# Kernel tuning notes

Measured on AMD Instinct MI355X. Metric: run time of the kernel, lower is better.

Reference implementation:

```python
import jax, jax.numpy as jnp
import numpy as np

B, DZ, DE, M, H = 4096, 2048, 128, 32, 1024
GATE_TEMP = 1.0


def setup_inputs() -> dict:
    key = jax.random.key(0)
    ks = jax.random.split(key, 6)
    s = lambda k, shape, sc: jax.random.normal(k, shape, dtype=jnp.float32) * sc
    return dict(
        z=s(ks[0], (B, DZ), 1.0),
        base_W=s(ks[1], (3, DZ), 0.02),
        base_b=jnp.zeros((3,), jnp.float32),
        gate_W=s(ks[2], (DE, DZ), 0.02),
        gate_b=jnp.zeros((DE,), jnp.float32),
        E=s(ks[3], (M, DE), 0.02),              # material embedding table
        W1=s(ks[4], (M, H, DZ + DE), 0.02),     # stacked first-layer weights
        b1=jnp.zeros((M, H), jnp.float32),
        W2=s(ks[5], (M, 3, H), 0.02),           # stacked second-layer weights
        b2=jnp.zeros((M, 3), jnp.float32),
    )


def _l2norm(x, eps=1e-12):
    # matches F.normalize(dim=-1): x / max(||x||_2, eps)
    n = jnp.linalg.norm(x, axis=-1, keepdims=True)
    return x / jnp.maximum(n, eps)


def reference(z, base_W, base_b, gate_W, gate_b, E, W1, b1, W2, b2):
    dz = z.shape[1]
    # base head: [B, 3]
    b = z @ base_W.T + base_b
    # gate similarities (routing logits): [B, M]
    q = _l2norm(z @ gate_W.T + gate_b)
    sims = q @ _l2norm(E).T
    # Per-material 2-layer MLP on cat([z, E_m]) fused as grouped GEMMs.
    # Split W1 into the z-part and embedding-part of the concat input.
    W1z, W1e = W1[:, :, :dz], W1[:, :, dz:]
    emb_term = jnp.einsum('me,mhe->mh', E, W1e)        # [M, H], shared across batch
    h = jax.nn.gelu(
        jnp.einsum('bi,mhi->bmh', z, W1z) + emb_term[None] + b1[None],
        approximate=False,
    )                                                   # [B, M, H]
    delta = jnp.einsum('bmh,moh->bmo', h, W2) + b2[None]  # [B, M, 3]
    # scale_delta_by_gate=False path; dropout inactive at inference.
    L = (b[:, None, :] + delta).reshape(z.shape[0], -1)   # [B, 3*M]
    return L, sims
```

## Files before the change

kernel.cpp:

```cpp
#include <hip/hip_runtime.h>
#include <hip/hip_bf16.h>
#include <math.h>

#define B_ROWS 4096
#define DZ     2048
#define DE     128
#define M_EXP  32
#define H_DIM  1024
#define NBIG   32768
#define NEXTRA 256
#define NTOT   (NBIG + NEXTRA)
#define W1_LD  (DZ + DE)

typedef _Float16 half8 __attribute__((ext_vector_type(8)));
typedef float    f32x4 __attribute__((ext_vector_type(4)));

#define AS1 __attribute__((address_space(1)))
#define AS3 __attribute__((address_space(3)))

__device__ __forceinline__ void async_copy16(const void* g, void* l) {
  __builtin_amdgcn_global_load_lds((const AS1 void*)g, (AS3 void*)l, 16, 0, 0);
}

__device__ __forceinline__ half8 cvt8(const float4& a, const float4& b) {
  half8 h = {(_Float16)a.x, (_Float16)a.y, (_Float16)a.z, (_Float16)a.w,
             (_Float16)b.x, (_Float16)b.y, (_Float16)b.z, (_Float16)b.w};
  return h;
}

__device__ __forceinline__ float gelu_f(float x) {
  float u = fabsf(x) * 0.70710678118654752f;
  float t = 1.0f / fmaf(0.3275911f, u, 1.0f);
  float poly = t * fmaf(t, fmaf(t, fmaf(t, fmaf(t, 1.061405429f, -1.453152027f),
                                        1.421413741f), -0.284496736f), 0.254829592f);
  float er = 1.0f - poly * __expf(-u * u);
  er = copysignf(er, x);
  return 0.5f * x * (1.0f + er);
}

__global__ __launch_bounds__(256) void k_cvt_z(const float* __restrict__ z,
                                               _Float16* __restrict__ zpk) {
  long g = (long)blockIdx.x * 256 + threadIdx.x;
  int row = (int)(g >> 8);
  int k0  = ((int)g & 255) * 8;
  float4 a = *(const float4*)(z + (long)row * DZ + k0);
  float4 b = *(const float4*)(z + (long)row * DZ + k0 + 4);
  int r16 = row >> 4, rl = row & 15, kt = k0 >> 5, lg = (k0 >> 3) & 3;
  long dst = ((long)(r16 * 64 + kt) << 9) + (rl + 16 * lg) * 8;
  *(half8*)(zpk + dst) = cvt8(a, b);
}

__global__ __launch_bounds__(256) void k_cvt_w1(const float* __restrict__ W1,
                                                const float* __restrict__ E,
                                                const float* __restrict__ b1,
                                                _Float16* __restrict__ W1h,
                                                float* __restrict__ hbias) {
  const long n = blockIdx.x;
  const int  t = threadIdx.x;
  const float* src = W1 + n * W1_LD;
  float4 a = *(const float4*)(src + t * 8);
  float4 b = *(const float4*)(src + t * 8 + 4);
  *(half8*)(W1h + n * DZ + t * 8) = cvt8(a, b);
  if (t < 32) {
    int m = (int)(n >> 10);
    float4 w = *(const float4*)(src + DZ + t * 4);
    float4 e = *(const float4*)(E + m * DE + t * 4);
    float p = w.x * e.x + w.y * e.y + w.z * e.z + w.w * e.w;
    p += __shfl_xor(p, 16);
    p += __shfl_xor(p, 8);
    p += __shfl_xor(p, 4);
    p += __shfl_xor(p, 2);
    p += __shfl_xor(p, 1);
    if (t == 0) hbias[n] = p + b1[n];
  }
}

__global__ __launch_bounds__(256) void k_cvt_small(const float* __restrict__ gate_W,
                                                   const float* __restrict__ base_W,
                                                   _Float16* __restrict__ W1h) {
  int r = blockIdx.x;
  int t = threadIdx.x;
  const float* src = nullptr;
  if (r < 128)       src = gate_W + (long)r * DZ;
  else if (r < 131)  src = base_W + (long)(r - 128) * DZ;
  _Float16* dst = W1h + (long)(NBIG + r) * DZ + t * 8;
  if (src) {
    float4 a = *(const float4*)(src + t * 8);
    float4 b = *(const float4*)(src + t * 8 + 4);
    *(half8*)dst = cvt8(a, b);
  } else {
    half8 zv = {(_Float16)0, (_Float16)0, (_Float16)0, (_Float16)0,
                (_Float16)0, (_Float16)0, (_Float16)0, (_Float16)0};
    *(half8*)dst = zv;
  }
}

__global__ __launch_bounds__(256, 2) void k_gemm(const _Float16* __restrict__ Apk,
                                                 const _Float16* __restrict__ Bm,
                                                 const float* __restrict__ hbias,
                                                 const float* __restrict__ W2,
                                                 float* __restrict__ Lout,
                                                 float* __restrict__ qraw) {
  __shared__ _Float16 sm[3][8192];

  int flat = blockIdx.y * gridDim.x + blockIdx.x;
  int wg   = (flat & 7) * 516 + (flat >> 3);
  const int tN = wg >> 5;
  const int tM = wg & 31;

  const int tid = threadIdx.x;
  const int w = tid >> 6, l = tid & 63;
  const int wm = w >> 1, wn = w & 1;
  const int rl = l & 15, lg = l >> 4;

  const int srow  = tid >> 2;
  const int sgoff = ((tid & 3) ^ ((srow >> 1) & 3)) * 8;
  const _Float16* gB = Bm + (long)(tN * 256 + srow) * DZ + sgoff;

#define STAGE_B(sb, kt) do { \
    async_copy16(gB + (kt) * 32,            &sm[sb][tid * 8]); \
    async_copy16(gB + 64 * DZ + (kt) * 32,  &sm[sb][2048 + tid * 8]); \
    async_copy16(gB + 128 * DZ + (kt) * 32, &sm[sb][4096 + tid * 8]); \
    async_copy16(gB + 192 * DZ + (kt) * 32, &sm[sb][6144 + tid * 8]); } while (0)

  const _Float16* gA = Apk + ((long)(tM * 8 + wm * 4) << 9) * 64 + l * 8;

#define RD_AG(dst, kt) do { _Pragma("unroll") for (int _i = 0; _i < 4; ++_i) \
    dst[_i] = *(const half8*)(gA + ((long)(_i * 64 + (kt)) << 9)); } while (0)

  const int aswz  = (lg ^ ((rl >> 1) & 3)) * 8;
  const int offB0 = (wn * 128 + rl) * 32 + aswz;

  half8 AFe[4], AFo[4], bf03[4], bf47[4];
  f32x4 acc[4][8];
  f32x4 z4 = {0.f, 0.f, 0.f, 0.f};
#pragma unroll
  for (int i = 0; i < 4; ++i)
#pragma unroll
    for (int j = 0; j < 8; ++j) acc[i][j] = z4;

#define RD_B(sl) do { \
    _Pragma("unroll") for (int _j = 0; _j < 4; ++_j) \
      bf03[_j] = *(const half8*)&sm[sl][offB0 + _j * 512]; \
    _Pragma("unroll") for (int _j = 0; _j < 4; ++_j) \
      bf47[_j] = *(const half8*)&sm[sl][offB0 + (4 + _j) * 512]; } while (0)

#define MFMA32(af_) do { \
    _Pragma("unroll") for (int _i = 0; _i < 4; ++_i) \
    _Pragma("unroll") for (int _j = 0; _j < 4; ++_j) \
      acc[_i][_j] = __builtin_amdgcn_mfma_f32_16x16x32_f16(af_[_i], bf03[_j], acc[_i][_j], 0, 0, 0); \
    _Pragma("unroll") for (int _i = 0; _i < 4; ++_i) \
    _Pragma("unroll") for (int _j = 0; _j < 4; ++_j) \
      acc[_i][4 + _j] = __builtin_amdgcn_mfma_f32_16x16x32_f16(af_[_i], bf47[_j], acc[_i][4 + _j], 0, 0, 0); \
  } while (0)

#define BAR() do { asm volatile("" ::: "memory"); __builtin_amdgcn_s_barrier(); asm volatile("" ::: "memory"); } while (0)
#define VM8 asm volatile("s_waitcnt vmcnt(8)" ::: "memory")
#define VM4 asm volatile("s_waitcnt vmcnt(4)" ::: "memory")
#define VM0 asm volatile("s_waitcnt vmcnt(0)" ::: "memory")

#define TILE_FULL(sl, s2, kt2, AFc, AFn, ktA) do { \
    BAR(); \
    RD_B(sl); \
    STAGE_B(s2, kt2); \
    RD_AG(AFn, ktA); \
    VM8; \
    MFMA32(AFc); } while (0)
#define TILE_A(sl, AFc, AFn, ktA, CERT) do { \
    BAR(); \
    RD_B(sl); \
    RD_AG(AFn, ktA); \
    CERT; \
    MFMA32(AFc); } while (0)
#define TILE_LAST(sl, AFc) do { \
    BAR(); \
    RD_B(sl); \
    VM0; \
    MFMA32(AFc); } while (0)

  STAGE_B(0, 0);
  STAGE_B(1, 1);
  RD_AG(AFe, 0);
  VM8;

#pragma unroll 1
  for (int n = 0; n < 10; ++n) {
    const int t6 = 6 * n;
    TILE_FULL(0, 2, t6 + 2, AFe, AFo, t6 + 1);
    TILE_FULL(1, 0, t6 + 3, AFo, AFe, t6 + 2);
    TILE_FULL(2, 1, t6 + 4, AFe, AFo, t6 + 3);
    TILE_FULL(0, 2, t6 + 5, AFo, AFe, t6 + 4);
    TILE_FULL(1, 0, t6 + 6, AFe, AFo, t6 + 5);
    TILE_FULL(2, 1, t6 + 7, AFo, AFe, t6 + 6);
  }
  TILE_FULL(0, 2, 62, AFe, AFo, 61);
  TILE_FULL(1, 0, 63, AFo, AFe, 62);
  TILE_A(2, AFe, AFo, 63, VM4);
  TILE_LAST(0, AFo);

  if (tN < 128) {
    const int m = tN >> 2;
    float hb[8], w2v[3][8];
#pragma unroll
    for (int j = 0; j < 8; ++j) {
      int gcol = tN * 256 + wn * 128 + j * 16 + rl;
      int he   = gcol & (H_DIM - 1);
      hb[j] = hbias[gcol];
#pragma unroll
      for (int o = 0; o < 3; ++o) w2v[o][j] = W2[((long)m * 3 + o) * H_DIM + he];
    }
#pragma unroll
    for (int i = 0; i < 4; ++i) {
      const int growb = tM * 128 + wm * 64 + i * 16 + lg * 4;
#pragma unroll
      for (int r = 0; r < 4; ++r) {
        int grow = growb + r;
        float hv[8];
#pragma unroll
        for (int j = 0; j < 8; ++j) hv[j] = gelu_f(acc[i][j][r] + hb[j]);
#pragma unroll
        for (int o = 0; o < 3; ++o) {
          float p = 0.f;
#pragma unroll
          for (int j = 0; j < 8; ++j) p = fmaf(hv[j], w2v[o][j], p);
          p += __shfl_xor(p, 1);
          p += __shfl_xor(p, 2);
          p += __shfl_xor(p, 4);
          p += __shfl_xor(p, 8);
          if (rl == o) atomicAdd(&Lout[(long)grow * 96 + m * 3 + o], p);
        }
      }
    }
  } else {
#pragma unroll
    for (int i = 0; i < 4; ++i) {
      const int growb = tM * 128 + wm * 64 + i * 16 + lg * 4;
#pragma unroll
      for (int r = 0; r < 4; ++r) {
        int grow = growb + r;
        int c0 = wn * 128 + rl;
#pragma unroll
        for (int j = 0; j < 8; ++j)
          qraw[(long)grow * 256 + c0 + j * 16] = acc[i][j][r];
      }
    }
  }
}

__global__ __launch_bounds__(128) void k_post(const float* __restrict__ qraw,
                                              const float* __restrict__ gate_b,
                                              const float* __restrict__ base_b,
                                              const float* __restrict__ E,
                                              const float* __restrict__ b2,
                                              float* __restrict__ out) {
  const int b = blockIdx.x;
  const int t = threadIdx.x;
  __shared__ float qs[DE];
  __shared__ float invE[M_EXP];
  __shared__ float wsum[2];
  __shared__ float pA[M_EXP], pB[M_EXP];

  if (t < 32) {
    float ss = 0.f;
    const float* er = E + t * DE;
    for (int e = 0; e < DE; ++e) { float v = er[e]; ss += v * v; }
    invE[t] = 1.0f / fmaxf(sqrtf(ss), 1e-12f);
  }

  float val = qraw[(long)b * 256 + t] + gate_b[t];
  float ss = val * val;
  ss += __shfl_xor(ss, 1);  ss += __shfl_xor(ss, 2);  ss += __shfl_xor(ss, 4);
  ss += __shfl_xor(ss, 8);  ss += __shfl_xor(ss, 16); ss += __shfl_xor(ss, 32);
  if ((t & 63) == 0) wsum[t >> 6] = ss;
  __syncthreads();
  float inv = 1.0f / fmaxf(sqrtf(wsum[0] + wsum[1]), 1e-12f);
  qs[t] = val * inv;
  __syncthreads();

  {
    int m = t & 31, hf = t >> 5;
    const float* er = E + m * DE + hf * 32;
    const float* qq = qs + hf * 32;
    float p = 0.f;
#pragma unroll
    for (int e = 0; e < 32; ++e) p += qq[e] * er[e];
    p += __shfl_xor(p, 32);
    if (t < 32) pA[m] = p;
    else if (t >= 64 && t < 96) pB[m] = p;
    __syncthreads();
    if (t < 32) out[(long)B_ROWS * 96 + (long)b * 32 + t] = (pA[t] + pB[t]) * invE[t];
  }

  if (t < 96) {
    int o = t % 3;
    float bv = qraw[(long)b * 256 + 128 + o] + base_b[o];
    out[(long)b * 96 + t] += bv + b2[t];
  }
}

extern "C" void kernel_launch(void* const* d_in, const int* in_sizes, int n_in,
                              void* d_out, int out_size, void* d_ws, size_t ws_size,
                              hipStream_t stream) {
  const float* z      = (const float*)d_in[0];
  const float* base_W = (const float*)d_in[1];
  const float* base_b = (const float*)d_in[2];
  const float* gate_W = (const float*)d_in[3];
  const float* gate_b = (const float*)d_in[4];
  const float* E      = (const float*)d_in[5];
  const float* W1     = (const float*)d_in[6];
  const float* b1     = (const float*)d_in[7];
  const float* W2     = (const float*)d_in[8];
  const float* b2     = (const float*)d_in[9];
  float* out = (float*)d_out;

  char* ws = (char*)d_ws;
  const size_t off_zh    = 0;
  const size_t off_w1h   = off_zh  + (size_t)B_ROWS * DZ * 2;
  const size_t off_hbias = off_w1h + (size_t)NTOT * DZ * 2;
  const size_t off_qraw  = off_hbias + (size_t)NBIG * 4;
  _Float16* zpk   = (_Float16*)(ws + off_zh);
  _Float16* W1h   = (_Float16*)(ws + off_w1h);
  float*    hbias = (float*)(ws + off_hbias);
  float*    qraw  = (float*)(ws + off_qraw);

  hipMemsetAsync(d_out, 0, (size_t)B_ROWS * 96 * sizeof(float), stream);

  k_cvt_z<<<(B_ROWS * DZ) / (256 * 8), 256, 0, stream>>>(z, zpk);
  k_cvt_w1<<<NBIG, 256, 0, stream>>>(W1, E, b1, W1h, hbias);
  k_cvt_small<<<NEXTRA, 256, 0, stream>>>(gate_W, base_W, W1h);
  k_gemm<<<dim3(129, 32), 256, 0, stream>>>(zpk, W1h, hbias, W2, out, qraw);
  k_post<<<B_ROWS, 128, 0, stream>>>(qraw, gate_b, base_b, E, b2, out);
}
```

Before: 761.3 us.

## Change warp tiling to 1x4 so each warp covers all 128 rows and 64 columns

```diff
diff --git a/kernel.cpp b/kernel.cpp
--- a/kernel.cpp
+++ b/kernel.cpp
@@ -109,8 +109,8 @@
   const int tM = wg & 31;
 
   const int tid = threadIdx.x;
-  const int w = tid >> 6, l = tid & 63;
-  const int wm = w >> 1, wn = w & 1;
+  const int wn = tid >> 6;
+  const int l = tid & 63;
   const int rl = l & 15, lg = l >> 4;
 
   const int srow  = tid >> 2;
@@ -123,48 +123,42 @@
     async_copy16(gB + 128 * DZ + (kt) * 32, &sm[sb][4096 + tid * 8]); \
     async_copy16(gB + 192 * DZ + (kt) * 32, &sm[sb][6144 + tid * 8]); } while (0)
 
-  const _Float16* gA = Apk + ((long)(tM * 8 + wm * 4) << 9) * 64 + l * 8;
-
-#define RD_AG(dst, kt) do { _Pragma("unroll") for (int _i = 0; _i < 4; ++_i) \
+  const _Float16* gA = Apk + (((long)(tM * 8)) << 9) * 64 + l * 8;
+
+#define RD_AG(dst, kt) do { _Pragma("unroll") for (int _i = 0; _i < 8; ++_i) \
     dst[_i] = *(const half8*)(gA + ((long)(_i * 64 + (kt)) << 9)); } while (0)
 
   const int aswz  = (lg ^ ((rl >> 1) & 3)) * 8;
-  const int offB0 = (wn * 128 + rl) * 32 + aswz;
-
-  half8 AFe[4], AFo[4], bf03[4], bf47[4];
-  f32x4 acc[4][8];
+  const int offB0 = (wn * 64 + rl) * 32 + aswz;
+
+  half8 AFe[8], AFo[8], bf[4];
+  f32x4 acc[8][4];
   f32x4 z4 = {0.f, 0.f, 0.f, 0.f};
 #pragma unroll
-  for (int i = 0; i < 4; ++i)
-#pragma unroll
-    for (int j = 0; j < 8; ++j) acc[i][j] = z4;
-
-#define RD_B(sl) do { \
+  for (int i = 0; i < 8; ++i)
+#pragma unroll
+    for (int j = 0; j < 4; ++j) acc[i][j] = z4;
+
+#define RD_B(sl) do { _Pragma("unroll") for (int _j = 0; _j < 4; ++_j) \
+    bf[_j] = *(const half8*)&sm[sl][offB0 + _j * 512]; } while (0)
+
+#define MFMA32(af_) do { \
+    _Pragma("unroll") for (int _i = 0; _i < 8; ++_i) \
     _Pragma("unroll") for (int _j = 0; _j < 4; ++_j) \
-      bf03[_j] = *(const half8*)&sm[sl][offB0 + _j * 512]; \
-    _Pragma("unroll") for (int _j = 0; _j < 4; ++_j) \
-      bf47[_j] = *(const half8*)&sm[sl][offB0 + (4 + _j) * 512]; } while (0)
-
-#define MFMA32(af_) do { \
-    _Pragma("unroll") for (int _i = 0; _i < 4; ++_i) \
-    _Pragma("unroll") for (int _j = 0; _j < 4; ++_j) \
-      acc[_i][_j] = __builtin_amdgcn_mfma_f32_16x16x32_f16(af_[_i], bf03[_j], acc[_i][_j], 0, 0, 0); \
-    _Pragma("unroll") for (int _i = 0; _i < 4; ++_i) \
-    _Pragma("unroll") for (int _j = 0; _j < 4; ++_j) \
-      acc[_i][4 + _j] = __builtin_amdgcn_mfma_f32_16x16x32_f16(af_[_i], bf47[_j], acc[_i][4 + _j], 0, 0, 0); \
+      acc[_i][_j] = __builtin_amdgcn_mfma_f32_16x16x32_f16(af_[_i], bf[_j], acc[_i][_j], 0, 0, 0); \
   } while (0)
 
 #define BAR() do { asm volatile("" ::: "memory"); __builtin_amdgcn_s_barrier(); asm volatile("" ::: "memory"); } while (0)
-#define VM8 asm volatile("s_waitcnt vmcnt(8)" ::: "memory")
-#define VM4 asm volatile("s_waitcnt vmcnt(4)" ::: "memory")
-#define VM0 asm volatile("s_waitcnt vmcnt(0)" ::: "memory")
+#define VM12 asm volatile("s_waitcnt vmcnt(12)" ::: "memory")
+#define VM8  asm volatile("s_waitcnt vmcnt(8)" ::: "memory")
+#define VM0  asm volatile("s_waitcnt vmcnt(0)" ::: "memory")
 
 #define TILE_FULL(sl, s2, kt2, AFc, AFn, ktA) do { \
     BAR(); \
     RD_B(sl); \
     STAGE_B(s2, kt2); \
     RD_AG(AFn, ktA); \
-    VM8; \
+    VM12; \
     MFMA32(AFc); } while (0)
 #define TILE_A(sl, AFc, AFn, ktA, CERT) do { \
     BAR(); \
@@ -181,7 +175,7 @@
   STAGE_B(0, 0);
   STAGE_B(1, 1);
   RD_AG(AFe, 0);
-  VM8;
+  VM12;
 
 #pragma unroll 1
   for (int n = 0; n < 10; ++n) {
@@ -195,34 +189,32 @@
   }
   TILE_FULL(0, 2, 62, AFe, AFo, 61);
   TILE_FULL(1, 0, 63, AFo, AFe, 62);
-  TILE_A(2, AFe, AFo, 63, VM4);
+  TILE_A(2, AFe, AFo, 63, VM8);
   TILE_LAST(0, AFo);
 
   if (tN < 128) {
     const int m = tN >> 2;
-    float hb[8], w2v[3][8];
-#pragma unroll
-    for (int j = 0; j < 8; ++j) {
-      int gcol = tN * 256 + wn * 128 + j * 16 + rl;
+    float hb[4], w2v[3][4];
+#pragma unroll
+    for (int j = 0; j < 4; ++j) {
+      int gcol = tN * 256 + wn * 64 + j * 16 + rl;
       int he   = gcol & (H_DIM - 1);
       hb[j] = hbias[gcol];
 #pragma unroll
       for (int o = 0; o < 3; ++o) w2v[o][j] = W2[((long)m * 3 + o) * H_DIM + he];
     }
 #pragma unroll
-    for (int i = 0; i < 4; ++i) {
-      const int growb = tM * 128 + wm * 64 + i * 16 + lg * 4;
+    for (int i = 0; i < 8; ++i) {
+      const int growb = tM * 128 + i * 16 + lg * 4;
 #pragma unroll
       for (int r = 0; r < 4; ++r) {
         int grow = growb + r;
-        float hv[8];
-#pragma unroll
-        for (int j = 0; j < 8; ++j) hv[j] = gelu_f(acc[i][j][r] + hb[j]);
+        float hv[4];
+#pragma unroll
+        for (int j = 0; j < 4; ++j) hv[j] = gelu_f(acc[i][j][r] + hb[j]);
 #pragma unroll
         for (int o = 0; o < 3; ++o) {
-          float p = 0.f;
-#pragma unroll
-          for (int j = 0; j < 8; ++j) p = fmaf(hv[j], w2v[o][j], p);
+          float p = hv[0] * w2v[o][0] + hv[1] * w2v[o][1] + hv[2] * w2v[o][2] + hv[3] * w2v[o][3];
           p += __shfl_xor(p, 1);
           p += __shfl_xor(p, 2);
           p += __shfl_xor(p, 4);
@@ -233,14 +225,14 @@
     }
   } else {
 #pragma unroll
-    for (int i = 0; i < 4; ++i) {
-      const int growb = tM * 128 + wm * 64 + i * 16 + lg * 4;
+    for (int i = 0; i < 8; ++i) {
+      const int growb = tM * 128 + i * 16 + lg * 4;
 #pragma unroll
       for (int r = 0; r < 4; ++r) {
         int grow = growb + r;
-        int c0 = wn * 128 + rl;
-#pragma unroll
-        for (int j = 0; j < 8; ++j)
+        int c0 = wn * 64 + rl;
+#pragma unroll
+        for (int j = 0; j < 4; ++j)
           qraw[(long)grow * 256 + c0 + j * 16] = acc[i][j][r];
       }
     }
```

Measured after the change: 862.5 us. +13.3%, slower.

## Pre-pack W1 into MFMA fragment layout and drop LDS staging in GEMM

Applied to the files above, without the earlier changes.

```diff
diff --git a/kernel.cpp b/kernel.cpp
--- a/kernel.cpp
+++ b/kernel.cpp
@@ -14,13 +14,6 @@
 
 typedef _Float16 half8 __attribute__((ext_vector_type(8)));
 typedef float    f32x4 __attribute__((ext_vector_type(4)));
-
-#define AS1 __attribute__((address_space(1)))
-#define AS3 __attribute__((address_space(3)))
-
-__device__ __forceinline__ void async_copy16(const void* g, void* l) {
-  __builtin_amdgcn_global_load_lds((const AS1 void*)g, (AS3 void*)l, 16, 0, 0);
-}
 
 __device__ __forceinline__ half8 cvt8(const float4& a, const float4& b) {
   half8 h = {(_Float16)a.x, (_Float16)a.y, (_Float16)a.z, (_Float16)a.w,
@@ -53,14 +46,16 @@
 __global__ __launch_bounds__(256) void k_cvt_w1(const float* __restrict__ W1,
                                                 const float* __restrict__ E,
                                                 const float* __restrict__ b1,
-                                                _Float16* __restrict__ W1h,
+                                                _Float16* __restrict__ Bpk,
                                                 float* __restrict__ hbias) {
   const long n = blockIdx.x;
   const int  t = threadIdx.x;
   const float* src = W1 + n * W1_LD;
   float4 a = *(const float4*)(src + t * 8);
   float4 b = *(const float4*)(src + t * 8 + 4);
-  *(half8*)(W1h + n * DZ + t * 8) = cvt8(a, b);
+  int n16 = (int)(n >> 4), nl = (int)(n & 15), kt = t >> 2, lg = t & 3;
+  long dst = ((long)(n16 * 64 + kt) << 9) + (nl + 16 * lg) * 8;
+  *(half8*)(Bpk + dst) = cvt8(a, b);
   if (t < 32) {
     int m = (int)(n >> 10);
     float4 w = *(const float4*)(src + DZ + t * 4);
@@ -77,32 +72,32 @@
 
 __global__ __launch_bounds__(256) void k_cvt_small(const float* __restrict__ gate_W,
                                                    const float* __restrict__ base_W,
-                                                   _Float16* __restrict__ W1h) {
+                                                   _Float16* __restrict__ Bpk) {
   int r = blockIdx.x;
   int t = threadIdx.x;
   const float* src = nullptr;
   if (r < 128)       src = gate_W + (long)r * DZ;
   else if (r < 131)  src = base_W + (long)(r - 128) * DZ;
-  _Float16* dst = W1h + (long)(NBIG + r) * DZ + t * 8;
+  long n = NBIG + r;
+  int n16 = (int)(n >> 4), nl = (int)(n & 15), kt = t >> 2, lg = t & 3;
+  long dsto = ((long)(n16 * 64 + kt) << 9) + (nl + 16 * lg) * 8;
   if (src) {
     float4 a = *(const float4*)(src + t * 8);
     float4 b = *(const float4*)(src + t * 8 + 4);
-    *(half8*)dst = cvt8(a, b);
+    *(half8*)(Bpk + dsto) = cvt8(a, b);
   } else {
     half8 zv = {(_Float16)0, (_Float16)0, (_Float16)0, (_Float16)0,
                 (_Float16)0, (_Float16)0, (_Float16)0, (_Float16)0};
-    *(half8*)dst = zv;
+    *(half8*)(Bpk + dsto) = zv;
   }
 }
 
 __global__ __launch_bounds__(256, 2) void k_gemm(const _Float16* __restrict__ Apk,
-                                                 const _Float16* __restrict__ Bm,
+                                                 const _Float16* __restrict__ Bpk,
                                                  const float* __restrict__ hbias,
                                                  const float* __restrict__ W2,
                                                  float* __restrict__ Lout,
                                                  float* __restrict__ qraw) {
-  __shared__ _Float16 sm[3][8192];
-
   int flat = blockIdx.y * gridDim.x + blockIdx.x;
   int wg   = (flat & 7) * 516 + (flat >> 3);
   const int tN = wg >> 5;
@@ -113,25 +108,15 @@
   const int wm = w >> 1, wn = w & 1;
   const int rl = l & 15, lg = l >> 4;
 
-  const int srow  = tid >> 2;
-  const int sgoff = ((tid & 3) ^ ((srow >> 1) & 3)) * 8;
-  const _Float16* gB = Bm + (long)(tN * 256 + srow) * DZ + sgoff;
-
-#define STAGE_B(sb, kt) do { \
-    async_copy16(gB + (kt) * 32,            &sm[sb][tid * 8]); \
-    async_copy16(gB + 64 * DZ + (kt) * 32,  &sm[sb][2048 + tid * 8]); \
-    async_copy16(gB + 128 * DZ + (kt) * 32, &sm[sb][4096 + tid * 8]); \
-    async_copy16(gB + 192 * DZ + (kt) * 32, &sm[sb][6144 + tid * 8]); } while (0)
-
-  const _Float16* gA = Apk + ((long)(tM * 8 + wm * 4) << 9) * 64 + l * 8;
-
-#define RD_AG(dst, kt) do { _Pragma("unroll") for (int _i = 0; _i < 4; ++_i) \
+  const _Float16* gA = Apk + (((long)(tM * 8  + wm * 4)) << 15) + l * 8;
+  const _Float16* gB = Bpk + (((long)(tN * 16 + wn * 8)) << 15) + l * 8;
+
+#define RD_A(dst, kt) do { _Pragma("unroll") for (int _i = 0; _i < 4; ++_i) \
     dst[_i] = *(const half8*)(gA + ((long)(_i * 64 + (kt)) << 9)); } while (0)
-
-  const int aswz  = (lg ^ ((rl >> 1) & 3)) * 8;
-  const int offB0 = (wn * 128 + rl) * 32 + aswz;
-
-  half8 AFe[4], AFo[4], bf03[4], bf47[4];
+#define RD_B(dst, kt) do { _Pragma("unroll") for (int _j = 0; _j < 8; ++_j) \
+    dst[_j] = *(const half8*)(gB + ((long)(_j * 64 + (kt)) << 9)); } while (0)
+
+  half8 aE[4], bE[8], aO[4], bO[8];
   f32x4 acc[4][8];
   f32x4 z4 = {0.f, 0.f, 0.f, 0.f};
 #pragma unroll
@@ -139,64 +124,23 @@
 #pragma unroll
     for (int j = 0; j < 8; ++j) acc[i][j] = z4;
 
-#define RD_B(sl) do { \
-    _Pragma("unroll") for (int _j = 0; _j < 4; ++_j) \
-      bf03[_j] = *(const half8*)&sm[sl][offB0 + _j * 512]; \
-    _Pragma("unroll") for (int _j = 0; _j < 4; ++_j) \
-      bf47[_j] = *(const half8*)&sm[sl][offB0 + (4 + _j) * 512]; } while (0)
-
-#define MFMA32(af_) do { \
+#define MFMA32(a_, b_) do { \
     _Pragma("unroll") for (int _i = 0; _i < 4; ++_i) \
-    _Pragma("unroll") for (int _j = 0; _j < 4; ++_j) \
-      acc[_i][_j] = __builtin_amdgcn_mfma_f32_16x16x32_f16(af_[_i], bf03[_j], acc[_i][_j], 0, 0, 0); \
-    _Pragma("unroll") for (int _i = 0; _i < 4; ++_i) \
-    _Pragma("unroll") for (int _j = 0; _j < 4; ++_j) \
-      acc[_i][4 + _j] = __builtin_amdgcn_mfma_f32_16x16x32_f16(af_[_i], bf47[_j], acc[_i][4 + _j], 0, 0, 0); \
+    _Pragma("unroll") for (int _j = 0; _j < 8; ++_j) \
+      acc[_i][_j] = __builtin_amdgcn_mfma_f32_16x16x32_f16(a_[_i], b_[_j], acc[_i][_j], 0, 0, 0); \
   } while (0)
 
-#define BAR() do { asm volatile("" ::: "memory"); __builtin_amdgcn_s_barrier(); asm volatile("" ::: "memory"); } while (0)
-#define VM8 asm volatile("s_waitcnt vmcnt(8)" ::: "memory")
-#define VM4 asm volatile("s_waitcnt vmcnt(4)" ::: "memory")
-#define VM0 asm volatile("s_waitcnt vmcnt(0)" ::: "memory")
-
-#define TILE_FULL(sl, s2, kt2, AFc, AFn, ktA) do { \
-    BAR(); \
-    RD_B(sl); \
-    STAGE_B(s2, kt2); \
-    RD_AG(AFn, ktA); \
-    VM8; \
-    MFMA32(AFc); } while (0)
-#define TILE_A(sl, AFc, AFn, ktA, CERT) do { \
-    BAR(); \
-    RD_B(sl); \
-    RD_AG(AFn, ktA); \
-    CERT; \
-    MFMA32(AFc); } while (0)
-#define TILE_LAST(sl, AFc) do { \
-    BAR(); \
-    RD_B(sl); \
-    VM0; \
-    MFMA32(AFc); } while (0)
-
-  STAGE_B(0, 0);
-  STAGE_B(1, 1);
-  RD_AG(AFe, 0);
-  VM8;
-
+  RD_A(aE, 0); RD_B(bE, 0);
 #pragma unroll 1
-  for (int n = 0; n < 10; ++n) {
-    const int t6 = 6 * n;
-    TILE_FULL(0, 2, t6 + 2, AFe, AFo, t6 + 1);
-    TILE_FULL(1, 0, t6 + 3, AFo, AFe, t6 + 2);
-    TILE_FULL(2, 1, t6 + 4, AFe, AFo, t6 + 3);
-    TILE_FULL(0, 2, t6 + 5, AFo, AFe, t6 + 4);
-    TILE_FULL(1, 0, t6 + 6, AFe, AFo, t6 + 5);
-    TILE_FULL(2, 1, t6 + 7, AFo, AFe, t6 + 6);
-  }
-  TILE_FULL(0, 2, 62, AFe, AFo, 61);
-  TILE_FULL(1, 0, 63, AFo, AFe, 62);
-  TILE_A(2, AFe, AFo, 63, VM4);
-  TILE_LAST(0, AFo);
+  for (int n = 0; n < 31; ++n) {
+    RD_A(aO, 2 * n + 1); RD_B(bO, 2 * n + 1);
+    MFMA32(aE, bE);
+    RD_A(aE, 2 * n + 2); RD_B(bE, 2 * n + 2);
+    MFMA32(aO, bO);
+  }
+  RD_A(aO, 63); RD_B(bO, 63);
+  MFMA32(aE, bE);
+  MFMA32(aO, bO);
 
   if (tN < 128) {
     const int m = tN >> 2;
@@ -319,15 +263,15 @@
   const size_t off_hbias = off_w1h + (size_t)NTOT * DZ * 2;
   const size_t off_qraw  = off_hbias + (size_t)NBIG * 4;
   _Float16* zpk   = (_Float16*)(ws + off_zh);
-  _Float16* W1h   = (_Float16*)(ws + off_w1h);
+  _Float16* Bpk   = (_Float16*)(ws + off_w1h);
   float*    hbias = (float*)(ws + off_hbias);
   float*    qraw  = (float*)(ws + off_qraw);
 
   hipMemsetAsync(d_out, 0, (size_t)B_ROWS * 96 * sizeof(float), stream);
 
   k_cvt_z<<<(B_ROWS * DZ) / (256 * 8), 256, 0, stream>>>(z, zpk);
-  k_cvt_w1<<<NBIG, 256, 0, stream>>>(W1, E, b1, W1h, hbias);
-  k_cvt_small<<<NEXTRA, 256, 0, stream>>>(gate_W, base_W, W1h);
-  k_gemm<<<dim3(129, 32), 256, 0, stream>>>(zpk, W1h, hbias, W2, out, qraw);
+  k_cvt_w1<<<NBIG, 256, 0, stream>>>(W1, E, b1, Bpk, hbias);
+  k_cvt_small<<<NEXTRA, 256, 0, stream>>>(gate_W, base_W, Bpk);
+  k_gemm<<<dim3(129, 32), 256, 0, stream>>>(zpk, Bpk, hbias, W2, out, qraw);
   k_post<<<B_ROWS, 128, 0, stream>>>(qraw, gate_b, base_b, E, b2, out);
 }
```

Result: slower. 919.1 us (+20.7%).

## Restructure GEMM main loop into two-tile phases with four LDS buffers

Applied to the files above, without the earlier changes.

```diff
diff --git a/kernel.cpp b/kernel.cpp
--- a/kernel.cpp
+++ b/kernel.cpp
@@ -101,7 +101,7 @@
                                                  const float* __restrict__ W2,
                                                  float* __restrict__ Lout,
                                                  float* __restrict__ qraw) {
-  __shared__ _Float16 sm[3][8192];
+  __shared__ _Float16 sm[4][8192];
 
   int flat = blockIdx.y * gridDim.x + blockIdx.x;
   int wg   = (flat & 7) * 516 + (flat >> 3);
@@ -131,7 +131,7 @@
   const int aswz  = (lg ^ ((rl >> 1) & 3)) * 8;
   const int offB0 = (wn * 128 + rl) * 32 + aswz;
 
-  half8 AFe[4], AFo[4], bf03[4], bf47[4];
+  half8 AFe[4], AFo[4], bf[8];
   f32x4 acc[4][8];
   f32x4 z4 = {0.f, 0.f, 0.f, 0.f};
 #pragma unroll
@@ -139,64 +139,61 @@
 #pragma unroll
     for (int j = 0; j < 8; ++j) acc[i][j] = z4;
 
-#define RD_B(sl) do { \
-    _Pragma("unroll") for (int _j = 0; _j < 4; ++_j) \
-      bf03[_j] = *(const half8*)&sm[sl][offB0 + _j * 512]; \
-    _Pragma("unroll") for (int _j = 0; _j < 4; ++_j) \
-      bf47[_j] = *(const half8*)&sm[sl][offB0 + (4 + _j) * 512]; } while (0)
+#define RD_B8(sl) do { _Pragma("unroll") for (int _j = 0; _j < 8; ++_j) \
+    bf[_j] = *(const half8*)&sm[sl][offB0 + _j * 512]; } while (0)
 
 #define MFMA32(af_) do { \
     _Pragma("unroll") for (int _i = 0; _i < 4; ++_i) \
-    _Pragma("unroll") for (int _j = 0; _j < 4; ++_j) \
-      acc[_i][_j] = __builtin_amdgcn_mfma_f32_16x16x32_f16(af_[_i], bf03[_j], acc[_i][_j], 0, 0, 0); \
-    _Pragma("unroll") for (int _i = 0; _i < 4; ++_i) \
-    _Pragma("unroll") for (int _j = 0; _j < 4; ++_j) \
-      acc[_i][4 + _j] = __builtin_amdgcn_mfma_f32_16x16x32_f16(af_[_i], bf47[_j], acc[_i][4 + _j], 0, 0, 0); \
+    _Pragma("unroll") for (int _j = 0; _j < 8; ++_j) \
+      acc[_i][_j] = __builtin_amdgcn_mfma_f32_16x16x32_f16(af_[_i], bf[_j], acc[_i][_j], 0, 0, 0); \
   } while (0)
 
 #define BAR() do { asm volatile("" ::: "memory"); __builtin_amdgcn_s_barrier(); asm volatile("" ::: "memory"); } while (0)
-#define VM8 asm volatile("s_waitcnt vmcnt(8)" ::: "memory")
-#define VM4 asm volatile("s_waitcnt vmcnt(4)" ::: "memory")
+#define SBAR0 __builtin_amdgcn_sched_barrier(0)
 #define VM0 asm volatile("s_waitcnt vmcnt(0)" ::: "memory")
 
-#define TILE_FULL(sl, s2, kt2, AFc, AFn, ktA) do { \
+#define PHASE(s0, kt) do { \
     BAR(); \
-    RD_B(sl); \
-    STAGE_B(s2, kt2); \
-    RD_AG(AFn, ktA); \
-    VM8; \
-    MFMA32(AFc); } while (0)
-#define TILE_A(sl, AFc, AFn, ktA, CERT) do { \
+    RD_B8(s0); \
+    STAGE_B((s0) ^ 2, (kt) + 2); \
+    STAGE_B(((s0) ^ 2) | 1, (kt) + 3); \
+    SBAR0; \
+    RD_AG(AFo, (kt) + 1); \
+    MFMA32(AFe); \
+    RD_AG(AFe, (kt) + 2); \
+    RD_B8((s0) | 1); \
+    MFMA32(AFo); } while (0)
+#define PHASE_S(s0, kt) do { \
     BAR(); \
-    RD_B(sl); \
-    RD_AG(AFn, ktA); \
-    CERT; \
-    MFMA32(AFc); } while (0)
-#define TILE_LAST(sl, AFc) do { \
+    RD_B8(s0); \
+    STAGE_B((s0) ^ 2, (kt) + 2); \
+    STAGE_B(((s0) ^ 2) | 1, (kt) + 3); \
+    SBAR0; \
+    RD_AG(AFo, (kt) + 1); \
+    MFMA32(AFe); \
+    RD_AG(AFe, (kt) + 2); \
+    RD_B8((s0) | 1); \
+    MFMA32(AFo); } while (0)
+#define PHASE_LAST(s0, kt) do { \
     BAR(); \
-    RD_B(sl); \
-    VM0; \
-    MFMA32(AFc); } while (0)
+    RD_B8(s0); \
+    RD_AG(AFo, (kt) + 1); \
+    MFMA32(AFe); \
+    RD_B8((s0) | 1); \
+    MFMA32(AFo); } while (0)
 
   STAGE_B(0, 0);
   STAGE_B(1, 1);
   RD_AG(AFe, 0);
-  VM8;
+  VM0;
 
 #pragma unroll 1
-  for (int n = 0; n < 10; ++n) {
-    const int t6 = 6 * n;
-    TILE_FULL(0, 2, t6 + 2, AFe, AFo, t6 + 1);
-    TILE_FULL(1, 0, t6 + 3, AFo, AFe, t6 + 2);
-    TILE_FULL(2, 1, t6 + 4, AFe, AFo, t6 + 3);
-    TILE_FULL(0, 2, t6 + 5, AFo, AFe, t6 + 4);
-    TILE_FULL(1, 0, t6 + 6, AFe, AFo, t6 + 5);
-    TILE_FULL(2, 1, t6 + 7, AFo, AFe, t6 + 6);
-  }
-  TILE_FULL(0, 2, 62, AFe, AFo, 61);
-  TILE_FULL(1, 0, 63, AFo, AFe, 62);
-  TILE_A(2, AFe, AFo, 63, VM4);
-  TILE_LAST(0, AFo);
+  for (int n = 0; n < 15; ++n) {
+    PHASE(0, 4 * n);
+    PHASE(2, 4 * n + 2);
+  }
+  PHASE_S(0, 60);
+  PHASE_LAST(2, 62);
 
   if (tN < 128) {
     const int m = tN >> 2;
```

Result: slower. 844.5 us (+10.9%).
